# Optimization experiments

Measured on AMD Instinct MI355X. Metric: run time of the kernel, lower is better.

## Reference

```python
import jax, jax.numpy as jnp
import numpy as np

B, T, C = 2, 4096, 768
H = 12
HD = C // H  # 64


def setup_inputs() -> dict:
    key = jax.random.key(0)
    k1, k2, k3 = jax.random.split(key, 3)
    scale = 0.02
    x = jax.random.normal(k1, (B, T, C), dtype=jnp.float32)
    w_attn = jax.random.normal(k2, (C, 3 * C), dtype=jnp.float32) * scale
    b_attn = jnp.zeros((3 * C,), dtype=jnp.float32)
    w_proj = jax.random.normal(k3, (C, C), dtype=jnp.float32) * scale
    b_proj = jnp.zeros((C,), dtype=jnp.float32)
    return {"x": x, "w_attn": w_attn, "b_attn": b_attn,
            "w_proj": w_proj, "b_proj": b_proj}


def reference(x, w_attn, b_attn, w_proj, b_proj):
    b, t, c = x.shape
    # QKV projection: (B,T,3C)
    qkv = x @ w_attn + b_attn
    q, k, v = jnp.split(qkv, 3, axis=2)
    # (B,H,T,HD)
    q = q.reshape(b, t, H, HD).transpose(0, 2, 1, 3)
    k = k.reshape(b, t, H, HD).transpose(0, 2, 1, 3)
    v = v.reshape(b, t, H, HD).transpose(0, 2, 1, 3)
    # scores: (B,H,T,T)
    scores = jnp.einsum('bhqd,bhkd->bhqk', q, k) / jnp.sqrt(jnp.float32(HD))
    causal = jnp.tril(jnp.ones((t, t), dtype=bool))
    scores = jnp.where(causal[None, None, :, :], scores, -jnp.inf)
    att = jax.nn.softmax(scores, axis=-1)
    # attn_dropout p=0 -> identity
    y = jnp.einsum('bhqk,bhkd->bhqd', att, v)
    y = y.transpose(0, 2, 1, 3).reshape(b, t, c)
    # output projection (resid_dropout p=0 -> identity)
    return y @ w_proj + b_proj
```

## Files before the change

kernel.cpp:

```cpp
#include <hip/hip_runtime.h>


typedef unsigned short u16;
typedef unsigned int u32;
using bf16x8 = __attribute__((ext_vector_type(8))) short;
using f32x4  = __attribute__((ext_vector_type(4))) float;

__device__ __forceinline__ float bf2f(u16 u) {
  return __uint_as_float(((u32)u) << 16);
}
__device__ __forceinline__ u16 f2bf(float f) {
  u32 u = __float_as_uint(f);
  u += 0x7fffu + ((u >> 16) & 1u);
  return (u16)(u >> 16);
}
__device__ __forceinline__ u32 cvtpk(float lo, float hi) {
  u32 r;
  asm("v_cvt_pk_bf16_f32 %0, %1, %2" : "=v"(r) : "v"(lo), "v"(hi));
  return r;
}
__device__ __forceinline__ void gload_lds16(const u16* g, u16* l) {
  __builtin_amdgcn_global_load_lds(
      (const __attribute__((address_space(1))) unsigned int*)g,
      (__attribute__((address_space(3))) unsigned int*)l, 16, 0, 0);
}

__global__ void fill_sentinel_f32(float* __restrict__ out, int n, float v) {
  const int i0 = blockIdx.x * blockDim.x + threadIdx.x;
  const int stride = gridDim.x * blockDim.x;
  for (int i = i0; i < n; i += stride) out[i] = v;
}

__global__ __launch_bounds__(256)
void prep(const float* __restrict__ x, const float* __restrict__ w_attn,
          const float* __restrict__ b_attn, const float* __restrict__ w_proj,
          const float* __restrict__ b_proj, u16* __restrict__ xb,
          u16* __restrict__ WtA, u16* __restrict__ WtP,
          u16* __restrict__ ba, u16* __restrict__ bp) {
  __shared__ u16 tile[32][33];
  const int bid = blockIdx.x, tid = threadIdx.x;
  if (bid < 2304) {
    const float* in; u16* out; int R, C, bx, by;
    if (bid < 1728) { in = w_attn; out = WtA; R = 768; C = 2304;
                      bx = bid % 72; by = bid / 72; }
    else            { in = w_proj; out = WtP; R = 768; C = 768;
                      bx = (bid - 1728) % 24; by = (bid - 1728) / 24; }
    const int c0 = bx * 32, r0 = by * 32;
    const int tx = tid & 31, ty = tid >> 5;
#pragma unroll
    for (int i = 0; i < 32; i += 8)
      tile[ty + i][tx] = f2bf(in[(size_t)(r0 + ty + i) * C + c0 + tx]);
    __syncthreads();
#pragma unroll
    for (int i = 0; i < 32; i += 8)
      out[(size_t)(c0 + ty + i) * R + r0 + tx] = tile[tx][ty + i];
  } else if (bid < 3328) {
    const int n4 = 8192 * 768 / 4;
    const int i0 = (bid - 2304) * 256 + tid, stride = 1024 * 256;
    const float4* src = (const float4*)x;
    ushort4* dst = (ushort4*)xb;
    for (int i = i0; i < n4; i += stride) {
      const float4 v = src[i];
      ushort4 o;
      o.x = f2bf(v.x); o.y = f2bf(v.y); o.z = f2bf(v.z); o.w = f2bf(v.w);
      dst[i] = o;
    }
  } else {
    for (int i = tid; i < 2304; i += 256) ba[i] = f2bf(b_attn[i]);
    for (int i = tid; i < 768; i += 256) bp[i] = f2bf(b_proj[i]);
  }
}

#define QSCALE 0.18033688011112f

template <int MODE>
__global__ __launch_bounds__(256, 3)
void gemm128(const u16* __restrict__ A, const u16* __restrict__ Bt,
             const u16* __restrict__ bias, void* __restrict__ O0v,
             u16* __restrict__ O1, u16* __restrict__ O2, int Kd) {
  __shared__ __align__(16) u16 As[128 * 64];
  __shared__ __align__(16) u16 Bs[128 * 64];
  const int tid = threadIdx.x;
  const int lane = tid & 63, wave = tid >> 6;
  const int wm = wave >> 1, wn = wave & 1;
  const int l16 = lane & 15, quad = lane >> 4;

  const u16* Ag0 = A + (size_t)blockIdx.x * 128 * Kd +
                   (size_t)(tid >> 3) * Kd + (tid & 7) * 8;
  const u16* Bg0 = Bt + (size_t)blockIdx.y * 128 * Kd +
                   (size_t)(tid >> 3) * Kd + (tid & 7) * 8;
  const int ldsb = wave * 512;

  f32x4 acc[4][4] = {};
  for (int kt = 0; kt < Kd; kt += 64) {
#pragma unroll
    for (int i = 0; i < 4; ++i) {
      gload_lds16(Ag0 + (size_t)i * 32 * Kd + kt, &As[i * 2048 + ldsb]);
      gload_lds16(Bg0 + (size_t)i * 32 * Kd + kt, &Bs[i * 2048 + ldsb]);
    }
    __syncthreads();
#pragma unroll
    for (int s = 0; s < 2; ++s) {
      bf16x8 af[4], bfr[4];
#pragma unroll
      for (int i = 0; i < 4; ++i) {
        const int m = wm * 64 + i * 16 + l16;
        af[i] = *(const bf16x8*)&As[m * 64 + (s * 4 + quad) * 8];
        const int n = wn * 64 + i * 16 + l16;
        bfr[i] = *(const bf16x8*)&Bs[n * 64 + (s * 4 + quad) * 8];
      }
#pragma unroll
      for (int i = 0; i < 4; ++i)
#pragma unroll
        for (int j = 0; j < 4; ++j)
          acc[i][j] = __builtin_amdgcn_mfma_f32_16x16x32_bf16(af[i], bfr[j],
                                                              acc[i][j], 0, 0, 0);
    }
    __syncthreads();
  }

#pragma unroll
  for (int i = 0; i < 4; ++i) {
    const int mbase = blockIdx.x * 128 + wm * 64 + i * 16 + quad * 4;
#pragma unroll
    for (int j = 0; j < 4; ++j) {
      const int nb = blockIdx.y * 128 + wn * 64 + j * 16;
      const int n = nb + l16;
      const float bv = bf2f(bias[n]);
      if (MODE == 0) {
        const int which = nb / 768;
        const int b = mbase >> 12, t = mbase & 4095;
        const int c = n - which * 768;
        const int h = c >> 6, d = c & 63;
        const size_t bh = (size_t)b * 12 + h;
        if (which == 0) {
#pragma unroll
          for (int r = 0; r < 4; ++r)
            ((u16*)O0v)[((bh * 4096 + t + r) << 6) + d] =
                f2bf((acc[i][j][r] + bv) * QSCALE);
        } else if (which == 1) {
#pragma unroll
          for (int r = 0; r < 4; ++r)
            O1[((bh * 4096 + t + r) << 6) + d] = f2bf(acc[i][j][r] + bv);
        } else {
          ushort4 pk;
          pk.x = f2bf(acc[i][j][0] + bv);
          pk.y = f2bf(acc[i][j][1] + bv);
          pk.z = f2bf(acc[i][j][2] + bv);
          pk.w = f2bf(acc[i][j][3] + bv);
          *(ushort4*)&O2[((bh << 6) + (size_t)d) * 4096 + t] = pk;
        }
      } else {
#pragma unroll
        for (int r = 0; r < 4; ++r)
          ((float*)O0v)[(size_t)(mbase + r) * 768 + n] = acc[i][j][r] + bv;
      }
    }
  }
}

__global__ __launch_bounds__(256, 3)
void attn_chunk(const u16* __restrict__ Q, const u16* __restrict__ K,
                const u16* __restrict__ Vt, u16* __restrict__ Y,
                u16* __restrict__ part_o, float* __restrict__ part_l) {
  const int idx = blockIdx.x;
  const int bh = idx % 24;
  const int cid = 79 - (idx / 24);
  int qt = 0, base = 0, nc = 1;
  for (int q = 0; q < 32; ++q) {
    const int c = (q >> 3) + 1;
    if (cid < base + c) { qt = q; nc = c; break; }
    base += c;
  }
  const int j = cid - base;
  const int Nt = 2 * qt + 2;
  const int kbeg = j * 16;
  const int kend = (kbeg + 16 < Nt) ? kbeg + 16 : Nt;
  const int q0 = qt * 128;
  const int b = bh / 12, h = bh % 12;
  const size_t ho = (size_t)bh * 4096 * 64;
  const u16* Qg = Q + ho + (size_t)q0 * 64;
  const u16* Kg = K + ho;
  const u16* Vg = Vt + ho;

  __shared__ __align__(16) u16 Ks[3][64 * 64];
  __shared__ __align__(16) u16 Vs[3][64 * 64];

  const int tid = threadIdx.x;
  const int lane = tid & 63, wave = tid >> 6;
  const int l16 = lane & 15, quad = lane >> 4;
  const int sw8 = (l16 & 7) * 8;

  const int rl = tid >> 3, m7 = tid & 7;
  const int cs = (m7 ^ (rl & 7)) * 8;
  const u16* kg0 = Kg + (size_t)rl * 64 + cs;
  const u16* vg0 = Vg + (size_t)rl * 4096 + cs;
  const int wb = wave * 512;

  bf16x8 qf[2][2];
#pragma unroll
  for (int rt = 0; rt < 2; ++rt)
#pragma unroll
    for (int s = 0; s < 2; ++s)
      qf[rt][s] = *(const bf16x8*)&Qg[(wave * 32 + rt * 16 + l16) * 64 + s * 32 + quad * 8];

  bf16x8 ones;
#pragma unroll
  for (int e = 0; e < 8; ++e) ones[e] = (short)0x3F80;

  f32x4 lacc[2] = {};
  f32x4 o[2][4] = {};

  auto stage = [&](int bf, int kt2) {
    const size_t ko = (size_t)kt2 * 4096;
    const int to = kt2 * 64;
    gload_lds16(kg0 + ko,               &Ks[bf][wb]);
    gload_lds16(kg0 + ko + 2048,        &Ks[bf][2048 + wb]);
    gload_lds16(vg0 + to,               &Vs[bf][wb]);
    gload_lds16(vg0 + to + 32 * 4096,   &Vs[bf][2048 + wb]);
  };

  const int ntt = kend - kbeg;
  stage(0, kbeg);
  if (ntt > 1) {
    stage(1, kbeg + 1);
    asm volatile("s_waitcnt vmcnt(4)" ::: "memory");
  } else {
    asm volatile("s_waitcnt vmcnt(0)" ::: "memory");
  }
  __builtin_amdgcn_sched_barrier(0);
  __builtin_amdgcn_s_barrier();
  int cur = 0;

  for (int kt2 = kbeg; kt2 < kend; ++kt2) {
    const int t0 = kt2 * 64;
    const bool pf = (kt2 + 2 < kend);
    if (pf) {
      int nb = cur + 2; if (nb >= 3) nb -= 3;
      stage(nb, kt2 + 2);
    }
    __builtin_amdgcn_sched_barrier(0);

    f32x4 sc[4][2] = {};
#pragma unroll
    for (int s = 0; s < 2; ++s) {
      bf16x8 kf[4];
#pragma unroll
      for (int nt = 0; nt < 4; ++nt)
        kf[nt] = *(const bf16x8*)&Ks[cur][(nt * 16 + l16) * 64 +
                                          ((s * 32 + quad * 8) ^ sw8)];
      __builtin_amdgcn_s_setprio(1);
#pragma unroll
      for (int nt = 0; nt < 4; ++nt)
#pragma unroll
        for (int rt = 0; rt < 2; ++rt)
          sc[nt][rt] = __builtin_amdgcn_mfma_f32_16x16x32_bf16(kf[nt], qf[rt][s],
                                                               sc[nt][rt], 0, 0, 0);
      __builtin_amdgcn_s_setprio(0);
    }

    u32 pw[4][2][2];
#pragma unroll
    for (int rt = 0; rt < 2; ++rt) {
      const int rowb = q0 + wave * 32 + rt * 16;
      if (t0 + 63 <= rowb) {
#pragma unroll
        for (int nt = 0; nt < 4; ++nt) {
          f32x4 p;
#pragma unroll
          for (int r = 0; r < 4; ++r)
            p[r] = __builtin_amdgcn_exp2f(sc[nt][rt][r]);
          pw[nt][rt][0] = cvtpk(p[0], p[1]);
          pw[nt][rt][1] = cvtpk(p[2], p[3]);
        }
      } else {
        const int qrow = rowb + l16;
#pragma unroll
        for (int nt = 0; nt < 4; ++nt) {
          f32x4 p;
#pragma unroll
          for (int r = 0; r < 4; ++r) {
            float pv = __builtin_amdgcn_exp2f(sc[nt][rt][r]);
            if (t0 + nt * 16 + quad * 4 + r > qrow) pv = 0.f;
            p[r] = pv;
          }
          pw[nt][rt][0] = cvtpk(p[0], p[1]);
          pw[nt][rt][1] = cvtpk(p[2], p[3]);
        }
      }
    }

#pragma unroll
    for (int s2 = 0; s2 < 2; ++s2) {
      bf16x8 vf[4];
#pragma unroll
      for (int dt = 0; dt < 4; ++dt) {
        const int vbase = (dt * 16 + l16) * 64;
        const int a1 = vbase + ((s2 * 32 + quad * 4) ^ sw8);
        union { uint2 hv[2]; bf16x8 v; } uv;
        uv.hv[0] = *(const uint2*)&Vs[cur][a1];
        uv.hv[1] = *(const uint2*)&Vs[cur][a1 ^ 16];
        vf[dt] = uv.v;
      }
#pragma unroll
      for (int rt = 0; rt < 2; ++rt) {
        union { u32 w[4]; bf16x8 v; } up;
        up.w[0] = pw[2 * s2][rt][0];
        up.w[1] = pw[2 * s2][rt][1];
        up.w[2] = pw[2 * s2 + 1][rt][0];
        up.w[3] = pw[2 * s2 + 1][rt][1];
        __builtin_amdgcn_s_setprio(1);
#pragma unroll
        for (int dt = 0; dt < 4; ++dt)
          o[rt][dt] = __builtin_amdgcn_mfma_f32_16x16x32_bf16(up.v, vf[dt],
                                                              o[rt][dt], 0, 0, 0);
        lacc[rt] = __builtin_amdgcn_mfma_f32_16x16x32_bf16(up.v, ones,
                                                           lacc[rt], 0, 0, 0);
        __builtin_amdgcn_s_setprio(0);
      }
    }

    if (kt2 + 1 < kend) {
      if (pf) asm volatile("s_waitcnt vmcnt(4)" ::: "memory");
      else    asm volatile("s_waitcnt vmcnt(0)" ::: "memory");
      __builtin_amdgcn_sched_barrier(0);
      __builtin_amdgcn_s_barrier();
      if (++cur == 3) cur = 0;
    }
  }

  if (nc == 1) {
#pragma unroll
    for (int rt = 0; rt < 2; ++rt)
#pragma unroll
      for (int r = 0; r < 4; ++r) {
        const float inv = 1.f / lacc[rt][r];
        const int t = q0 + wave * 32 + rt * 16 + quad * 4 + r;
#pragma unroll
        for (int dt = 0; dt < 4; ++dt)
          Y[((size_t)b * 4096 + t) * 768 + h * 64 + dt * 16 + l16] =
              f2bf(o[rt][dt][r] * inv);
      }
  } else {
    const int pslot = bh * 72 + (cid - 8);
    u16* po = part_o + (size_t)pslot * 8192;
    float* pl = part_l + pslot * 128;
#pragma unroll
    for (int rt = 0; rt < 2; ++rt)
#pragma unroll
      for (int r = 0; r < 4; ++r) {
        const int row = wave * 32 + rt * 16 + quad * 4 + r;
#pragma unroll
        for (int dt = 0; dt < 4; ++dt)
          po[row * 64 + dt * 16 + l16] = f2bf(o[rt][dt][r]);
        if (l16 == 0) pl[row] = lacc[rt][r];
      }
  }
}

__global__ __launch_bounds__(256, 8)
void attn_combine(const u16* __restrict__ part_o, const float* __restrict__ part_l,
                  u16* __restrict__ Y) {
  const int bh = blockIdx.x, qt = 8 + blockIdx.y;
  const int g = qt >> 3, i = qt & 7;
  const int nc = g + 1;
  const int base = 4 * g * (g + 1) + i * (g + 1);
  const int slot0 = bh * 72 + base - 8;
  const int b = bh / 12, h = bh % 12;
  const int q0 = qt * 128;
  for (int e = threadIdx.x; e < 8192; e += 256) {
    const int row = e >> 6, d = e & 63;
    float Os = 0.f, ls = 0.f;
    for (int c = 0; c < nc; ++c) {
      Os += bf2f(part_o[(size_t)(slot0 + c) * 8192 + e]);
      ls += part_l[(slot0 + c) * 128 + row];
    }
    Y[((size_t)b * 4096 + q0 + row) * 768 + h * 64 + d] = f2bf(Os / ls);
  }
}

extern "C" void kernel_launch(void* const* d_in, const int* in_sizes, int n_in,
                              void* d_out, int out_size, void* d_ws, size_t ws_size,
                              hipStream_t stream) {
  (void)in_sizes; (void)n_in;
  const float* x      = (const float*)d_in[0];
  const float* w_attn = (const float*)d_in[1];
  const float* b_attn = (const float*)d_in[2];
  const float* w_proj = (const float*)d_in[3];
  const float* b_proj = (const float*)d_in[4];
  float* out = (float*)d_out;

  char* ws = (char*)d_ws;
  size_t off = 0;
  auto alloc = [&](size_t bytes) -> void* {
    void* p = ws + off;
    off += (bytes + 255) & ~(size_t)255;
    return p;
  };
  u16* xb  = (u16*)alloc((size_t)8192 * 768 * 2);
  u16* WtA = (u16*)alloc((size_t)2304 * 768 * 2);
  u16* WtP = (u16*)alloc((size_t)768 * 768 * 2);
  u16* ba  = (u16*)alloc(2304 * 2);
  u16* bp  = (u16*)alloc(768 * 2);
  u16* Q   = (u16*)alloc((size_t)6291456 * 2);
  u16* Kp  = (u16*)alloc((size_t)6291456 * 2);
  u16* Vt  = (u16*)alloc((size_t)6291456 * 2);
  u16* Y   = (u16*)alloc((size_t)6291456 * 2);
  u16* part_o  = (u16*)alloc((size_t)24 * 72 * 8192 * 2);
  float* part_l = (float*)alloc((size_t)24 * 72 * 128 * 4);

  if (ws_size < off) {
    fill_sentinel_f32<<<256, 256, 0, stream>>>(out, out_size,
                                               100.0f + (float)(ws_size >> 20));
    return;
  }

  prep<<<3329, 256, 0, stream>>>(x, w_attn, b_attn, w_proj, b_proj,
                                 xb, WtA, WtP, ba, bp);
  gemm128<0><<<dim3(64, 18), 256, 0, stream>>>(xb, WtA, ba, Q, Kp, Vt, 768);
  attn_chunk<<<1920, 256, 0, stream>>>(Q, Kp, Vt, Y, part_o, part_l);
  attn_combine<<<dim3(24, 24), 256, 0, stream>>>(part_o, part_l, Y);
  gemm128<1><<<dim3(64, 6), 256, 0, stream>>>(Y, WtP, bp, out, nullptr, nullptr, 768);
}
```

Baseline: 269.2 us.

## Use 256-row query tiles with 8-wave attention blocks and XCD-swizzle GEMM tiles

Attention blocks grow to 512 threads (8 waves), each handling a 256-row query tile. Each K/V tile in LDS is therefore shared by twice as many query rows, and each thread issues half as many staging loads. The chunk schedule, the partial-result slots and the combine kernel are reworked for the coarser tiling, which halves the number of attention blocks. The two GEMMs also get a block-index swizzle that spreads neighbouring tiles across the 8 XCDs for better L2 locality. The risks are lower occupancy, fewer blocks to balance load, and index errors in the new chunk and slot arithmetic.

```diff
diff --git a/kernel.cpp b/kernel.cpp
--- a/kernel.cpp
+++ b/kernel.cpp
@@ -73,7 +73,7 @@
 
 #define QSCALE 0.18033688011112f
 
-template <int MODE>
+template <int MODE, int NBX, int NWG>
 __global__ __launch_bounds__(256, 3)
 void gemm128(const u16* __restrict__ A, const u16* __restrict__ Bt,
              const u16* __restrict__ bias, void* __restrict__ O0v,
@@ -85,9 +85,13 @@
   const int wm = wave >> 1, wn = wave & 1;
   const int l16 = lane & 15, quad = lane >> 4;
 
-  const u16* Ag0 = A + (size_t)blockIdx.x * 128 * Kd +
+  const int d0 = blockIdx.y * NBX + blockIdx.x;
+  const int swz = (d0 & 7) * (NWG / 8) + (d0 >> 3);
+  const int bx = swz % NBX, by = swz / NBX;
+
+  const u16* Ag0 = A + (size_t)bx * 128 * Kd +
                    (size_t)(tid >> 3) * Kd + (tid & 7) * 8;
-  const u16* Bg0 = Bt + (size_t)blockIdx.y * 128 * Kd +
+  const u16* Bg0 = Bt + (size_t)by * 128 * Kd +
                    (size_t)(tid >> 3) * Kd + (tid & 7) * 8;
   const int ldsb = wave * 512;
 
@@ -121,10 +125,10 @@
 
 #pragma unroll
   for (int i = 0; i < 4; ++i) {
-    const int mbase = blockIdx.x * 128 + wm * 64 + i * 16 + quad * 4;
+    const int mbase = bx * 128 + wm * 64 + i * 16 + quad * 4;
 #pragma unroll
     for (int j = 0; j < 4; ++j) {
-      const int nb = blockIdx.y * 128 + wn * 64 + j * 16;
+      const int nb = by * 128 + wn * 64 + j * 16;
       const int n = nb + l16;
       const float bv = bf2f(bias[n]);
       if (MODE == 0) {
@@ -159,24 +163,24 @@
   }
 }
 
-__global__ __launch_bounds__(256, 3)
+__global__ __launch_bounds__(512, 4)
 void attn_chunk(const u16* __restrict__ Q, const u16* __restrict__ K,
                 const u16* __restrict__ Vt, u16* __restrict__ Y,
                 u16* __restrict__ part_o, float* __restrict__ part_l) {
   const int idx = blockIdx.x;
   const int bh = idx % 24;
-  const int cid = 79 - (idx / 24);
+  const int cid = 39 - (idx / 24);
   int qt = 0, base = 0, nc = 1;
-  for (int q = 0; q < 32; ++q) {
-    const int c = (q >> 3) + 1;
+  for (int q = 0; q < 16; ++q) {
+    const int c = (q >> 2) + 1;
     if (cid < base + c) { qt = q; nc = c; break; }
     base += c;
   }
   const int j = cid - base;
-  const int Nt = 2 * qt + 2;
+  const int Nt = 4 * qt + 4;
   const int kbeg = j * 16;
   const int kend = (kbeg + 16 < Nt) ? kbeg + 16 : Nt;
-  const int q0 = qt * 128;
+  const int q0 = qt * 256;
   const int b = bh / 12, h = bh % 12;
   const size_t ho = (size_t)bh * 4096 * 64;
   const u16* Qg = Q + ho + (size_t)q0 * 64;
@@ -212,19 +216,15 @@
   f32x4 o[2][4] = {};
 
   auto stage = [&](int bf, int kt2) {
-    const size_t ko = (size_t)kt2 * 4096;
-    const int to = kt2 * 64;
-    gload_lds16(kg0 + ko,               &Ks[bf][wb]);
-    gload_lds16(kg0 + ko + 2048,        &Ks[bf][2048 + wb]);
-    gload_lds16(vg0 + to,               &Vs[bf][wb]);
-    gload_lds16(vg0 + to + 32 * 4096,   &Vs[bf][2048 + wb]);
+    gload_lds16(kg0 + (size_t)kt2 * 4096, &Ks[bf][wb]);
+    gload_lds16(vg0 + kt2 * 64,           &Vs[bf][wb]);
   };
 
   const int ntt = kend - kbeg;
   stage(0, kbeg);
   if (ntt > 1) {
     stage(1, kbeg + 1);
-    asm volatile("s_waitcnt vmcnt(4)" ::: "memory");
+    asm volatile("s_waitcnt vmcnt(2)" ::: "memory");
   } else {
     asm volatile("s_waitcnt vmcnt(0)" ::: "memory");
   }
@@ -321,7 +321,7 @@
     }
 
     if (kt2 + 1 < kend) {
-      if (pf) asm volatile("s_waitcnt vmcnt(4)" ::: "memory");
+      if (pf) asm volatile("s_waitcnt vmcnt(2)" ::: "memory");
       else    asm volatile("s_waitcnt vmcnt(0)" ::: "memory");
       __builtin_amdgcn_sched_barrier(0);
       __builtin_amdgcn_s_barrier();
@@ -342,9 +342,9 @@
               f2bf(o[rt][dt][r] * inv);
       }
   } else {
-    const int pslot = bh * 72 + (cid - 8);
-    u16* po = part_o + (size_t)pslot * 8192;
-    float* pl = part_l + pslot * 128;
+    const int pslot = bh * 36 + (cid - 4);
+    u16* po = part_o + (size_t)pslot * 16384;
+    float* pl = part_l + pslot * 256;
 #pragma unroll
     for (int rt = 0; rt < 2; ++rt)
 #pragma unroll
@@ -361,19 +361,19 @@
 __global__ __launch_bounds__(256, 8)
 void attn_combine(const u16* __restrict__ part_o, const float* __restrict__ part_l,
                   u16* __restrict__ Y) {
-  const int bh = blockIdx.x, qt = 8 + blockIdx.y;
-  const int g = qt >> 3, i = qt & 7;
-  const int nc = g + 1;
-  const int base = 4 * g * (g + 1) + i * (g + 1);
-  const int slot0 = bh * 72 + base - 8;
+  const int bh = blockIdx.x, qt = 4 + blockIdx.y;
+  const int a = qt >> 2, bq = qt & 3;
+  const int nc = a + 1;
+  const int base = qt + 2 * a * (a - 1) + a * bq;
+  const int slot0 = bh * 36 + base - 4;
   const int b = bh / 12, h = bh % 12;
-  const int q0 = qt * 128;
-  for (int e = threadIdx.x; e < 8192; e += 256) {
+  const int q0 = qt * 256;
+  for (int e = threadIdx.x; e < 16384; e += 256) {
     const int row = e >> 6, d = e & 63;
     float Os = 0.f, ls = 0.f;
     for (int c = 0; c < nc; ++c) {
-      Os += bf2f(part_o[(size_t)(slot0 + c) * 8192 + e]);
-      ls += part_l[(slot0 + c) * 128 + row];
+      Os += bf2f(part_o[(size_t)(slot0 + c) * 16384 + e]);
+      ls += part_l[(slot0 + c) * 256 + row];
     }
     Y[((size_t)b * 4096 + q0 + row) * 768 + h * 64 + d] = f2bf(Os / ls);
   }
@@ -406,8 +406,8 @@
   u16* Kp  = (u16*)alloc((size_t)6291456 * 2);
   u16* Vt  = (u16*)alloc((size_t)6291456 * 2);
   u16* Y   = (u16*)alloc((size_t)6291456 * 2);
-  u16* part_o  = (u16*)alloc((size_t)24 * 72 * 8192 * 2);
-  float* part_l = (float*)alloc((size_t)24 * 72 * 128 * 4);
+  u16* part_o  = (u16*)alloc((size_t)24 * 36 * 16384 * 2);
+  float* part_l = (float*)alloc((size_t)24 * 36 * 256 * 4);
 
   if (ws_size < off) {
     fill_sentinel_f32<<<256, 256, 0, stream>>>(out, out_size,
@@ -417,8 +417,8 @@
 
   prep<<<3329, 256, 0, stream>>>(x, w_attn, b_attn, w_proj, b_proj,
                                  xb, WtA, WtP, ba, bp);
-  gemm128<0><<<dim3(64, 18), 256, 0, stream>>>(xb, WtA, ba, Q, Kp, Vt, 768);
-  attn_chunk<<<1920, 256, 0, stream>>>(Q, Kp, Vt, Y, part_o, part_l);
-  attn_combine<<<dim3(24, 24), 256, 0, stream>>>(part_o, part_l, Y);
-  gemm128<1><<<dim3(64, 6), 256, 0, stream>>>(Y, WtP, bp, out, nullptr, nullptr, 768);
-}
+  gemm128<0, 64, 1152><<<dim3(64, 18), 256, 0, stream>>>(xb, WtA, ba, Q, Kp, Vt, 768);
+  attn_chunk<<<960, 512, 0, stream>>>(Q, Kp, Vt, Y, part_o, part_l);
+  attn_combine<<<dim3(24, 12), 256, 0, stream>>>(part_o, part_l, Y);
+  gemm128<1, 64, 384><<<dim3(64, 6), 256, 0, stream>>>(Y, WtP, bp, out, nullptr, nullptr, 768);
+}
```

After: 315.0 us. 1.17x slower.
